# Kernel optimization log

Measured on AMD Instinct MI355X. Metric: run time of the kernel, lower is better.

Reference implementation:

```python
import jax, jax.numpy as jnp
import numpy as np

N = 100_000   # nodes
E = 1_600_000 # edges
IN, H, OUT = 128, 128, 128
G = 64        # graphs in batch
EPS = 1e-5    # batchnorm eps


def setup_inputs() -> dict:
    key = jax.random.key(0)
    ks = jax.random.split(key, 16)
    x = jax.random.normal(ks[0], (N, IN), dtype=jnp.float32)
    edge_index = jax.random.randint(ks[1], (2, E), 0, N, dtype=jnp.int32)
    batch = jnp.sort(jax.random.randint(ks[2], (N,), 0, G, dtype=jnp.int32))
    def lin(k, fi, fo):
        return jax.random.normal(k, (fi, fo), dtype=jnp.float32) / np.sqrt(fi).astype(np.float32)
    inp = {
        'x': x, 'edge_index': edge_index, 'batch': batch,
        'W1': lin(ks[3], IN, H), 'b1': jnp.zeros((H,), jnp.float32),
        'g1': jnp.ones((H,), jnp.float32), 'beta1': jnp.zeros((H,), jnp.float32),
        'W2': lin(ks[4], H, H), 'b2': jnp.zeros((H,), jnp.float32),
        'g2': jnp.ones((H,), jnp.float32), 'beta2': jnp.zeros((H,), jnp.float32),
        'W3': lin(ks[5], H, H), 'b3': jnp.zeros((H,), jnp.float32),
        'g3': jnp.ones((H,), jnp.float32), 'beta3': jnp.zeros((H,), jnp.float32),
        'fc_w': lin(ks[6], H, OUT), 'fc_b': jnp.zeros((OUT,), jnp.float32),
    }
    return inp


def _gcn_prep(edge_index):
    # add self loops, compute symmetric normalization (shared across layers)
    loop = jnp.arange(N, dtype=edge_index.dtype)
    row = jnp.concatenate([edge_index[0], loop])  # source
    col = jnp.concatenate([edge_index[1], loop])  # target
    deg = jax.ops.segment_sum(jnp.ones_like(col, dtype=jnp.float32), col, num_segments=N)
    dinv = jnp.where(deg > 0, jax.lax.rsqrt(deg), 0.0)
    norm = dinv[row] * dinv[col]  # (E+N,)
    return row, col, norm


def _gcn_bn_relu(h, W, b, g, beta, row, col, norm):
    hw = h @ W                                           # (N, H)
    msg = norm[:, None] * hw[row]                        # gather + scale
    h = jax.ops.segment_sum(msg, col, num_segments=N) + b  # scatter-add
    # BatchNorm1d (training-mode batch statistics, biased var)
    mu = jnp.mean(h, axis=0)
    var = jnp.mean(jnp.square(h - mu), axis=0)
    h = g * (h - mu) * jax.lax.rsqrt(var + EPS) + beta
    return jax.nn.relu(h)


def reference(x, edge_index, batch, W1, b1, g1, beta1, W2, b2, g2, beta2,
              W3, b3, g3, beta3, fc_w, fc_b):
    row, col, norm = _gcn_prep(edge_index)
    h = _gcn_bn_relu(x, W1, b1, g1, beta1, row, col, norm)
    h = _gcn_bn_relu(h, W2, b2, g2, beta2, row, col, norm)
    h = _gcn_bn_relu(h, W3, b3, g3, beta3, row, col, norm)
    # global_mean_pool over batch assignment
    sums = jax.ops.segment_sum(h, batch, num_segments=G)
    cnt = jax.ops.segment_sum(jnp.ones((N,), jnp.float32), batch, num_segments=G)
    pooled = sums / jnp.maximum(cnt, 1.0)[:, None]       # (G, H)
    return pooled @ fc_w + fc_b                          # (G, OUT)
```

## Files before the change

### kernel.cpp

```cpp
#include <hip/hip_runtime.h>

#define NN 100000
#define EE 1600000
#define HH 128
#define GG 64
#define TOT (EE + NN)
#define PSPLIT 8
#define NB 782
#define BCAP 4096
#define FCHUNK 4096

typedef __attribute__((ext_vector_type(8))) short s16x8;
typedef __attribute__((ext_vector_type(4))) float f32x4;

__device__ __forceinline__ unsigned short f2bf(float f) {
    unsigned u = __float_as_uint(f);
    u = u + 0x7FFFu + ((u >> 16) & 1u);
    return (unsigned short)(u >> 16);
}


__global__ __launch_bounds__(256) void setup_kernel(const float* __restrict__ x,
                                                    const int* __restrict__ batch,
                                                    const float* __restrict__ W0,
                                                    const float* __restrict__ W1,
                                                    const float* __restrict__ W2,
                                                    unsigned* __restrict__ Xbf,
                                                    int* __restrict__ cursor,
                                                    int* __restrict__ gstart, int* __restrict__ gend,
                                                    float* __restrict__ poolsum,
                                                    unsigned short* __restrict__ Wt) {
    int i = blockIdx.x * 256 + threadIdx.x;
    if (i < NN * 64) {
        float2 v = ((const float2*)x)[i];
        Xbf[i] = (unsigned)f2bf(v.x) | ((unsigned)f2bf(v.y) << 16);
    }
    if (i < NB) cursor[i] = i * BCAP;
    if (i < GG * HH) poolsum[i] = 0.f;
    if (i < GG) {
        int lo = 0, hi = NN;
        while (lo < hi) { int m = (lo + hi) >> 1; if (batch[m] < i) lo = m + 1; else hi = m; }
        int s = lo;
        lo = 0; hi = NN;
        while (lo < hi) { int m = (lo + hi) >> 1; if (batch[m] < i + 1) lo = m + 1; else hi = m; }
        gstart[i] = s;
        gend[i] = lo;
    }
    if (i < 3 * HH * HH) {
        int l = i >> 14, r = i & 16383;
        const float* W = (l == 0) ? W0 : (l == 1) ? W1 : W2;
        int k = r >> 7, n = r & 127;
        Wt[l * HH * HH + n * HH + k] = f2bf(W[r]);
    }
}

__global__ __launch_bounds__(256) void bfill2_kernel(const int* __restrict__ ei, int* cursor,
                                                     unsigned* __restrict__ ebuf) {
    __shared__ int h[NB];
    __shared__ int lbase[NB];
    int tid = threadIdx.x;
    size_t e0 = (size_t)blockIdx.x * FCHUNK;
    for (int i = tid; i < NB; i += 256) h[i] = 0;
    __syncthreads();
    unsigned r[16], c[16];
#pragma unroll
    for (int k = 0; k < 16; ++k) {
        size_t e = e0 + (size_t)k * 256 + tid;
        unsigned rr = 0xFFFFFFFFu, cc = 0;
        if (e < EE) {
            rr = (unsigned)ei[e];
            cc = (unsigned)ei[EE + e];
            if (rr >= NN || cc >= NN) rr = 0xFFFFFFFFu;
        }
        r[k] = rr; c[k] = cc;
        if (rr != 0xFFFFFFFFu) atomicAdd(&h[cc >> 7], 1);
    }
    __syncthreads();
    for (int i = tid; i < NB; i += 256) {
        int cnt = h[i];
        lbase[i] = cnt ? atomicAdd(&cursor[i], cnt) : 0;
    }
    __syncthreads();
    for (int i = tid; i < NB; i += 256) h[i] = 0;
    __syncthreads();
#pragma unroll
    for (int k = 0; k < 16; ++k) {
        if (r[k] != 0xFFFFFFFFu) {
            unsigned cc = c[k];
            int b = cc >> 7;
            int slot = lbase[b] + atomicAdd(&h[b], 1);
            if (slot >= b * BCAP && slot < (b + 1) * BCAP)
                ebuf[slot] = (r[k] << 7) | (cc & 127u);
        }
    }
}

__global__ void bscan_kernel(const int* __restrict__ cursor, int* __restrict__ bucketSlotStart,
                             int* __restrict__ col_start) {
    __shared__ int ss[1024];
    int t = threadIdx.x;
    int ec = 0, nc = 0;
    if (t < NB) {
        ec = min(max(cursor[t] - t * BCAP, 0), BCAP);
        nc = min(128, NN - t * 128);
    }
    ss[t] = ec + nc;
    __syncthreads();
    for (int off = 1; off < 1024; off <<= 1) {
        int a = 0;
        if (t >= off) a = ss[t - off];
        __syncthreads();
        ss[t] += a;
        __syncthreads();
    }
    if (t < NB) bucketSlotStart[t] = ss[t] - (ec + nc);
    if (t == NB - 1) col_start[NN] = ss[t];
}

__global__ __launch_bounds__(256) void bproc_kernel(const unsigned* __restrict__ ebuf,
                                                    const int* __restrict__ cursor,
                                                    const int* __restrict__ bucketSlotStart,
                                                    int* __restrict__ col_start,
                                                    float* __restrict__ dinv,
                                                    int* __restrict__ srcv) {
    __shared__ unsigned s_e[BCAP];
    __shared__ int s_cnt[128], s_scan[128], s_cur[128];
    int b = blockIdx.x;
    int tid = threadIdx.x;
    int n0 = b * 128;
    int nb = min(128, NN - n0);
    int est = b * BCAP;
    int ecnt = min(max(cursor[b] - est, 0), BCAP);
    if (tid < 128) s_cnt[tid] = 0;
    __syncthreads();
    for (int i = tid; i < ecnt; i += 256) {
        unsigned v = ebuf[est + i];
        s_e[i] = v;
        atomicAdd(&s_cnt[v & 127u], 1);
    }
    __syncthreads();
    int myc = 0;
    if (tid < 128) {
        myc = (tid < nb) ? s_cnt[tid] + 1 : 0;
        s_scan[tid] = myc;
    }
    __syncthreads();
    for (int off = 1; off < 128; off <<= 1) {
        int a = 0;
        if (tid < 128 && tid >= off) a = s_scan[tid - off];
        __syncthreads();
        if (tid < 128) s_scan[tid] += a;
        __syncthreads();
    }
    if (tid < nb) {
        int slotbase = bucketSlotStart[b] + s_scan[tid] - myc;
        col_start[n0 + tid] = slotbase;
        dinv[n0 + tid] = rsqrtf((float)(s_cnt[tid] + 1));
        srcv[slotbase] = n0 + tid;
        s_cur[tid] = slotbase + 1;
    }
    __syncthreads();
    for (int i = tid; i < ecnt; i += 256) {
        unsigned v = s_e[i];
        int slot = atomicAdd(&s_cur[v & 127u], 1);
        srcv[slot] = (int)(v >> 7);
    }
}


__global__ __launch_bounds__(256) void agg_kernel(const uint4* __restrict__ Xbf4,
                                                  const int* __restrict__ col_start,
                                                  const int* __restrict__ srcv,
                                                  const float* __restrict__ dinv,
                                                  unsigned short* __restrict__ Abf,
                                                  float* __restrict__ gsum,
                                                  float* __restrict__ gsq) {
    if (blockIdx.x == 0 && threadIdx.x < HH) {
        gsum[threadIdx.x] = 0.f;
        gsq[threadIdx.x] = 0.f;
    }
    int wid = (int)((blockIdx.x * blockDim.x + threadIdx.x) >> 6);
    int lane = threadIdx.x & 63;
    if (wid >= NN) return;
    int s0 = col_start[wid], s1 = col_start[wid + 1];
    float dd = dinv[wid];
    int q = lane >> 4;
    int l16 = lane & 15;
    float acc[8];
#pragma unroll
    for (int j = 0; j < 8; ++j) acc[j] = 0.f;

    for (int base = s0; base < s1; base += 64) {
        int cnt = min(64, s1 - base);
        int msrc = 0;
        float mw = 0.f;
        if (lane < cnt) { msrc = srcv[base + lane]; mw = dinv[msrc] * dd; }
        int rounds = (cnt + 3) >> 2;
        int p = 0;
        for (; p + 4 <= rounds; p += 4) {
            uint4 u[4];
            float w[4];
#pragma unroll
            for (int k = 0; k < 4; ++k) {
                int idx = (p + k) * 4 + q;
                int src = __shfl(msrc, idx);
                w[k] = __shfl(mw, idx);
                u[k] = Xbf4[(size_t)src * 16 + l16];
            }
#pragma unroll
            for (int k = 0; k < 4; ++k) {
                acc[0] += w[k] * __uint_as_float(u[k].x << 16);
                acc[1] += w[k] * __uint_as_float(u[k].x & 0xFFFF0000u);
                acc[2] += w[k] * __uint_as_float(u[k].y << 16);
                acc[3] += w[k] * __uint_as_float(u[k].y & 0xFFFF0000u);
                acc[4] += w[k] * __uint_as_float(u[k].z << 16);
                acc[5] += w[k] * __uint_as_float(u[k].z & 0xFFFF0000u);
                acc[6] += w[k] * __uint_as_float(u[k].w << 16);
                acc[7] += w[k] * __uint_as_float(u[k].w & 0xFFFF0000u);
            }
        }
        for (; p < rounds; ++p) {
            int idx = p * 4 + q;
            int src = __shfl(msrc, idx);
            float w = __shfl(mw, idx);
            uint4 u = Xbf4[(size_t)src * 16 + l16];
            acc[0] += w * __uint_as_float(u.x << 16);
            acc[1] += w * __uint_as_float(u.x & 0xFFFF0000u);
            acc[2] += w * __uint_as_float(u.y << 16);
            acc[3] += w * __uint_as_float(u.y & 0xFFFF0000u);
            acc[4] += w * __uint_as_float(u.z << 16);
            acc[5] += w * __uint_as_float(u.z & 0xFFFF0000u);
            acc[6] += w * __uint_as_float(u.w << 16);
            acc[7] += w * __uint_as_float(u.w & 0xFFFF0000u);
        }
    }
#pragma unroll
    for (int j = 0; j < 8; ++j) {
        acc[j] += __shfl_xor(acc[j], 16);
        acc[j] += __shfl_xor(acc[j], 32);
    }
    if (q == 0) {
        uint4 pk;
        pk.x = (unsigned)f2bf(acc[0]) | ((unsigned)f2bf(acc[1]) << 16);
        pk.y = (unsigned)f2bf(acc[2]) | ((unsigned)f2bf(acc[3]) << 16);
        pk.z = (unsigned)f2bf(acc[4]) | ((unsigned)f2bf(acc[5]) << 16);
        pk.w = (unsigned)f2bf(acc[6]) | ((unsigned)f2bf(acc[7]) << 16);
        ((uint4*)Abf)[(size_t)wid * 16 + l16] = pk;
    }
}

__global__ __launch_bounds__(256) void gemm_stats_kernel(unsigned short* __restrict__ Abf,
                                                         const unsigned short* __restrict__ Wt,
                                                         const float* __restrict__ bias,
                                                         float* __restrict__ gsum,
                                                         float* __restrict__ gsq) {
    __shared__ unsigned short wlds[128 * 136];
    __shared__ float ssum[HH], ssq[HH];
    int tid = threadIdx.x;
    if (tid < HH) { ssum[tid] = 0.f; ssq[tid] = 0.f; }
#pragma unroll
    for (int it = 0; it < 16; ++it) {
        int idx = it * 256 + tid;
        int r = idx >> 5, c = idx & 31;
        *(uint2*)&wlds[r * 136 + c * 4] = *(const uint2*)(Wt + r * HH + c * 4);
    }
    __syncthreads();

    int lane = tid & 63;
    int wave = tid >> 6;
    int mcol = lane & 15;
    int quad = lane >> 4;
    int rowbase = blockIdx.x * 128 + wave * 32;
    int row0 = rowbase + mcol;
    int row1 = row0 + 16;

    f32x4 acc[2][8];
#pragma unroll
    for (int mt = 0; mt < 2; ++mt)
#pragma unroll
        for (int nt = 0; nt < 8; ++nt) acc[mt][nt] = (f32x4){0.f, 0.f, 0.f, 0.f};

    s16x8 zf = {0, 0, 0, 0, 0, 0, 0, 0};
#pragma unroll
    for (int ks = 0; ks < 4; ++ks) {
        int k0 = ks * 32 + quad * 8;
        s16x8 a0 = (row0 < NN) ? *(const s16x8*)(Abf + (size_t)row0 * HH + k0) : zf;
        s16x8 a1 = (row1 < NN) ? *(const s16x8*)(Abf + (size_t)row1 * HH + k0) : zf;
#pragma unroll
        for (int nt = 0; nt < 8; ++nt) {
            s16x8 b = *(const s16x8*)&wlds[(nt * 16 + mcol) * 136 + k0];
            acc[0][nt] = __builtin_amdgcn_mfma_f32_16x16x32_bf16(a0, b, acc[0][nt], 0, 0, 0);
            acc[1][nt] = __builtin_amdgcn_mfma_f32_16x16x32_bf16(a1, b, acc[1][nt], 0, 0, 0);
        }
    }

    float s[8], sq[8];
#pragma unroll
    for (int nt = 0; nt < 8; ++nt) { s[nt] = 0.f; sq[nt] = 0.f; }
#pragma unroll
    for (int mt = 0; mt < 2; ++mt) {
        int rbase = rowbase + mt * 16 + quad * 4;
#pragma unroll
        for (int nt = 0; nt < 8; ++nt) {
            int col = nt * 16 + mcol;
            float bv = bias[col];
            f32x4 a = acc[mt][nt];
#pragma unroll
            for (int reg = 0; reg < 4; ++reg) {
                int r = rbase + reg;
                if (r < NN) {
                    float h = a[reg] + bv;
                    Abf[(size_t)r * HH + col] = f2bf(h);
                    s[nt] += h; sq[nt] += h * h;
                }
            }
        }
    }
#pragma unroll
    for (int nt = 0; nt < 8; ++nt) {
        float v = s[nt];  v += __shfl_xor(v, 16);  v += __shfl_xor(v, 32);
        float w = sq[nt]; w += __shfl_xor(w, 16);  w += __shfl_xor(w, 32);
        if (quad == 0) {
            atomicAdd(&ssum[nt * 16 + mcol], v);
            atomicAdd(&ssq[nt * 16 + mcol], w);
        }
    }
    __syncthreads();
    if (tid < HH) {
        atomicAdd(&gsum[tid], ssum[tid]);
        atomicAdd(&gsq[tid], ssq[tid]);
    }
}

__global__ __launch_bounds__(256) void apply_kernel(const unsigned short* __restrict__ Hb,
                                                    const float* __restrict__ gsum,
                                                    const float* __restrict__ gsq,
                                                    const float* __restrict__ g,
                                                    const float* __restrict__ beta,
                                                    unsigned short* __restrict__ Xb16) {
    __shared__ float asc[HH], bsh[HH];
    int tid = threadIdx.x;
    if (tid < HH) {
        float mu = gsum[tid] * (1.f / (float)NN);
        float var = fmaxf(gsq[tid] * (1.f / (float)NN) - mu * mu, 0.f);
        float a = g[tid] * rsqrtf(var + 1e-5f);
        asc[tid] = a;
        bsh[tid] = beta[tid] - a * mu;
    }
    __syncthreads();
    int i = blockIdx.x * 256 + tid;
    if (i >= NN * 16) return;
    int c8 = (i & 15) * 8;
    uint4 u = ((const uint4*)Hb)[i];
    unsigned w[4] = {u.x, u.y, u.z, u.w};
    unsigned r[4];
#pragma unroll
    for (int k = 0; k < 4; ++k) {
        int c = c8 + 2 * k;
        float h0 = __uint_as_float(w[k] << 16);
        float h1 = __uint_as_float(w[k] & 0xFFFF0000u);
        float o0 = fmaxf(asc[c] * h0 + bsh[c], 0.f);
        float o1 = fmaxf(asc[c + 1] * h1 + bsh[c + 1], 0.f);
        r[k] = (unsigned)f2bf(o0) | ((unsigned)f2bf(o1) << 16);
    }
    uint4 o;
    o.x = r[0]; o.y = r[1]; o.z = r[2]; o.w = r[3];
    ((uint4*)Xb16)[i] = o;
}


__global__ void pool_kernel(const unsigned* __restrict__ Xbf, const int* __restrict__ gstart,
                            const int* __restrict__ gend, float* __restrict__ poolsum) {
    int g = blockIdx.x;
    int sp = blockIdx.y;
    int t = threadIdx.x;
    int s = gstart[g], e = gend[g];
    if (e <= s) return;
    int len = e - s;
    int chunk = (len + PSPLIT - 1) / PSPLIT;
    int cs = s + sp * chunk;
    int ce = min(cs + chunk, e);
    if (cs >= ce) return;
    float2 acc = make_float2(0.f, 0.f);
    for (int i = cs; i < ce; ++i) {
        unsigned u = Xbf[(size_t)i * 64 + t];
        acc.x += __uint_as_float(u << 16);
        acc.y += __uint_as_float(u & 0xFFFF0000u);
    }
    atomicAdd(&poolsum[g * HH + 2 * t], acc.x);
    atomicAdd(&poolsum[g * HH + 2 * t + 1], acc.y);
}

__global__ void fc_kernel(const float* __restrict__ poolsum, const int* __restrict__ gstart,
                          const int* __restrict__ gend, const float* __restrict__ fc_w,
                          const float* __restrict__ fc_b, float* __restrict__ out) {
    int g = blockIdx.x;
    int o = threadIdx.x;
    int cnt = gend[g] - gstart[g];
    float inv = (cnt > 0) ? (1.f / (float)cnt) : 0.f;
    float acc = fc_b[o];
    for (int k = 0; k < HH; ++k) acc += (poolsum[g * HH + k] * inv) * fc_w[k * HH + o];
    out[g * HH + o] = acc;
}


extern "C" void kernel_launch(void* const* d_in, const int* in_sizes, int n_in,
                              void* d_out, int out_size, void* d_ws, size_t ws_size,
                              hipStream_t stream) {
    const float* x     = (const float*)d_in[0];
    const int*   ei    = (const int*)d_in[1];
    const int*   batch = (const int*)d_in[2];
    const float* Wl[3]    = {(const float*)d_in[3], (const float*)d_in[7], (const float*)d_in[11]};
    const float* bl[3]    = {(const float*)d_in[4], (const float*)d_in[8], (const float*)d_in[12]};
    const float* gl[3]    = {(const float*)d_in[5], (const float*)d_in[9], (const float*)d_in[13]};
    const float* betal[3] = {(const float*)d_in[6], (const float*)d_in[10], (const float*)d_in[14]};
    const float* fc_w = (const float*)d_in[15];
    const float* fc_b = (const float*)d_in[16];
    float* out = (float*)d_out;

    char* ws = (char*)d_ws;
    size_t off = 0;
    auto take = [&](size_t n) -> void* {
        void* p = ws + off;
        off = (off + n + 255) & ~(size_t)255;
        return p;
    };
    int*   bucketSlotStart = (int*)take((size_t)NB * 4);
    int*   cursor          = (int*)take((size_t)NB * 4);
    unsigned* ebuf         = (unsigned*)take((size_t)NB * BCAP * 4);
    int*   col_start       = (int*)take((size_t)(NN + 1) * 4);
    float* dinv            = (float*)take((size_t)NN * 4);
    int*   srcv            = (int*)take((size_t)TOT * 4);
    float* gsum            = (float*)take(HH * 4);
    float* gsq             = (float*)take(HH * 4);
    int*   gstart          = (int*)take(GG * 4);
    int*   gend            = (int*)take(GG * 4);
    float* poolsum         = (float*)take((size_t)GG * HH * 4);
    unsigned short* wt     = (unsigned short*)take((size_t)3 * HH * HH * 2);
    unsigned* Xbf          = (unsigned*)take((size_t)NN * 64 * 4);
    unsigned short* Abf    = (unsigned short*)take((size_t)NN * HH * 2);

    setup_kernel<<<(NN * 64 + 255) / 256, 256, 0, stream>>>(x, batch, Wl[0], Wl[1], Wl[2],
                                                            Xbf, cursor, gstart, gend, poolsum, wt);
    bfill2_kernel<<<(EE + FCHUNK - 1) / FCHUNK, 256, 0, stream>>>(ei, cursor, ebuf);
    bscan_kernel<<<1, 1024, 0, stream>>>(cursor, bucketSlotStart, col_start);
    bproc_kernel<<<NB, 256, 0, stream>>>(ebuf, cursor, bucketSlotStart, col_start, dinv, srcv);

    for (int l = 0; l < 3; ++l) {
        const unsigned short* W = wt + (size_t)l * HH * HH;
        agg_kernel<<<(NN * 64 + 255) / 256, 256, 0, stream>>>((const uint4*)Xbf, col_start, srcv,
                                                              dinv, Abf, gsum, gsq);
        gemm_stats_kernel<<<(NN + 127) / 128, 256, 0, stream>>>(Abf, W, bl[l], gsum, gsq);
        apply_kernel<<<(NN * 16 + 255) / 256, 256, 0, stream>>>(Abf, gsum, gsq,
                                                                gl[l], betal[l],
                                                                (unsigned short*)Xbf);
    }

    pool_kernel<<<dim3(GG, PSPLIT), 64, 0, stream>>>(Xbf, gstart, gend, poolsum);
    fc_kernel<<<GG, 128, 0, stream>>>(poolsum, gstart, gend, fc_w, fc_b, out);
}
```

Before: 585.5 us.

## Recompute GEMM in fused BN-apply kernel and process two nodes per wave in aggregation

The aggregation kernel now has each 64-lane wave handle two destination nodes, 32 lanes each, and unrolls the gather six deep instead of four. This targets idle lanes on low-degree nodes and raises loads in flight. The stats GEMM no longer writes its pre-norm output. A new gemm_apply kernel recomputes the same GEMM and applies BatchNorm and ReLU in its epilogue, removing one bf16 write and read of the N×128 activation. The price is doing the MFMA GEMM twice per layer.

```diff
diff --git a/kernel.cpp b/kernel.cpp
--- a/kernel.cpp
+++ b/kernel.cpp
@@ -179,36 +179,41 @@
         gsum[threadIdx.x] = 0.f;
         gsq[threadIdx.x] = 0.f;
     }
-    int wid = (int)((blockIdx.x * blockDim.x + threadIdx.x) >> 6);
+    int wv = (int)((blockIdx.x * blockDim.x + threadIdx.x) >> 6);
     int lane = threadIdx.x & 63;
-    if (wid >= NN) return;
-    int s0 = col_start[wid], s1 = col_start[wid + 1];
-    float dd = dinv[wid];
-    int q = lane >> 4;
+    int half = lane >> 5;
+    int node = 2 * wv + half;
+    if (2 * wv >= NN) return;
+    bool valid = node < NN;
+    int s0 = 0, s1 = 0;
+    float dd = 0.f;
+    if (valid) { s0 = col_start[node]; s1 = col_start[node + 1]; dd = dinv[node]; }
+    int lane31 = lane & 31;
+    int qh = (lane >> 4) & 1;
     int l16 = lane & 15;
     float acc[8];
 #pragma unroll
     for (int j = 0; j < 8; ++j) acc[j] = 0.f;
 
-    for (int base = s0; base < s1; base += 64) {
-        int cnt = min(64, s1 - base);
+    for (int base = s0; base < s1; base += 32) {
+        int cnt = min(32, s1 - base);
         int msrc = 0;
         float mw = 0.f;
-        if (lane < cnt) { msrc = srcv[base + lane]; mw = dinv[msrc] * dd; }
-        int rounds = (cnt + 3) >> 2;
+        if (lane31 < cnt) { msrc = srcv[base + lane31]; mw = dinv[msrc] * dd; }
+        int rounds = (cnt + 1) >> 1;
         int p = 0;
-        for (; p + 4 <= rounds; p += 4) {
-            uint4 u[4];
-            float w[4];
-#pragma unroll
-            for (int k = 0; k < 4; ++k) {
-                int idx = (p + k) * 4 + q;
-                int src = __shfl(msrc, idx);
-                w[k] = __shfl(mw, idx);
+        for (; p + 6 <= rounds; p += 6) {
+            uint4 u[6];
+            float w[6];
+#pragma unroll
+            for (int k = 0; k < 6; ++k) {
+                int sl = half * 32 + (p + k) * 2 + qh;
+                int src = __shfl(msrc, sl);
+                w[k] = __shfl(mw, sl);
                 u[k] = Xbf4[(size_t)src * 16 + l16];
             }
 #pragma unroll
-            for (int k = 0; k < 4; ++k) {
+            for (int k = 0; k < 6; ++k) {
                 acc[0] += w[k] * __uint_as_float(u[k].x << 16);
                 acc[1] += w[k] * __uint_as_float(u[k].x & 0xFFFF0000u);
                 acc[2] += w[k] * __uint_as_float(u[k].y << 16);
@@ -220,9 +225,9 @@
             }
         }
         for (; p < rounds; ++p) {
-            int idx = p * 4 + q;
-            int src = __shfl(msrc, idx);
-            float w = __shfl(mw, idx);
+            int sl = half * 32 + p * 2 + qh;
+            int src = __shfl(msrc, sl);
+            float w = __shfl(mw, sl);
             uint4 u = Xbf4[(size_t)src * 16 + l16];
             acc[0] += w * __uint_as_float(u.x << 16);
             acc[1] += w * __uint_as_float(u.x & 0xFFFF0000u);
@@ -235,21 +240,18 @@
         }
     }
 #pragma unroll
-    for (int j = 0; j < 8; ++j) {
-        acc[j] += __shfl_xor(acc[j], 16);
-        acc[j] += __shfl_xor(acc[j], 32);
-    }
-    if (q == 0) {
+    for (int j = 0; j < 8; ++j) acc[j] += __shfl_xor(acc[j], 16);
+    if ((lane & 16) == 0 && valid) {
         uint4 pk;
         pk.x = (unsigned)f2bf(acc[0]) | ((unsigned)f2bf(acc[1]) << 16);
         pk.y = (unsigned)f2bf(acc[2]) | ((unsigned)f2bf(acc[3]) << 16);
         pk.z = (unsigned)f2bf(acc[4]) | ((unsigned)f2bf(acc[5]) << 16);
         pk.w = (unsigned)f2bf(acc[6]) | ((unsigned)f2bf(acc[7]) << 16);
-        ((uint4*)Abf)[(size_t)wid * 16 + l16] = pk;
-    }
-}
-
-__global__ __launch_bounds__(256) void gemm_stats_kernel(unsigned short* __restrict__ Abf,
+        ((uint4*)Abf)[(size_t)node * 16 + l16] = pk;
+    }
+}
+
+__global__ __launch_bounds__(256) void gemm_stats_kernel(const unsigned short* __restrict__ Abf,
                                                          const unsigned short* __restrict__ Wt,
                                                          const float* __restrict__ bias,
                                                          float* __restrict__ gsum,
@@ -302,15 +304,12 @@
         int rbase = rowbase + mt * 16 + quad * 4;
 #pragma unroll
         for (int nt = 0; nt < 8; ++nt) {
-            int col = nt * 16 + mcol;
-            float bv = bias[col];
+            float bv = bias[nt * 16 + mcol];
             f32x4 a = acc[mt][nt];
 #pragma unroll
             for (int reg = 0; reg < 4; ++reg) {
-                int r = rbase + reg;
-                if (r < NN) {
+                if (rbase + reg < NN) {
                     float h = a[reg] + bv;
-                    Abf[(size_t)r * HH + col] = f2bf(h);
                     s[nt] += h; sq[nt] += h * h;
                 }
             }
@@ -332,40 +331,78 @@
     }
 }
 
-__global__ __launch_bounds__(256) void apply_kernel(const unsigned short* __restrict__ Hb,
-                                                    const float* __restrict__ gsum,
-                                                    const float* __restrict__ gsq,
-                                                    const float* __restrict__ g,
-                                                    const float* __restrict__ beta,
-                                                    unsigned short* __restrict__ Xb16) {
+__global__ __launch_bounds__(256) void gemm_apply_kernel(const unsigned short* __restrict__ Abf,
+                                                         const unsigned short* __restrict__ Wt,
+                                                         const float* __restrict__ bias,
+                                                         const float* __restrict__ gsum,
+                                                         const float* __restrict__ gsq,
+                                                         const float* __restrict__ g,
+                                                         const float* __restrict__ beta,
+                                                         unsigned short* __restrict__ Xb16) {
+    __shared__ unsigned short wlds[128 * 136];
     __shared__ float asc[HH], bsh[HH];
     int tid = threadIdx.x;
+#pragma unroll
+    for (int it = 0; it < 16; ++it) {
+        int idx = it * 256 + tid;
+        int r = idx >> 5, c = idx & 31;
+        *(uint2*)&wlds[r * 136 + c * 4] = *(const uint2*)(Wt + r * HH + c * 4);
+    }
     if (tid < HH) {
         float mu = gsum[tid] * (1.f / (float)NN);
         float var = fmaxf(gsq[tid] * (1.f / (float)NN) - mu * mu, 0.f);
         float a = g[tid] * rsqrtf(var + 1e-5f);
         asc[tid] = a;
-        bsh[tid] = beta[tid] - a * mu;
-    }
-    __syncthreads();
-    int i = blockIdx.x * 256 + tid;
-    if (i >= NN * 16) return;
-    int c8 = (i & 15) * 8;
-    uint4 u = ((const uint4*)Hb)[i];
-    unsigned w[4] = {u.x, u.y, u.z, u.w};
-    unsigned r[4];
-#pragma unroll
-    for (int k = 0; k < 4; ++k) {
-        int c = c8 + 2 * k;
-        float h0 = __uint_as_float(w[k] << 16);
-        float h1 = __uint_as_float(w[k] & 0xFFFF0000u);
-        float o0 = fmaxf(asc[c] * h0 + bsh[c], 0.f);
-        float o1 = fmaxf(asc[c + 1] * h1 + bsh[c + 1], 0.f);
-        r[k] = (unsigned)f2bf(o0) | ((unsigned)f2bf(o1) << 16);
-    }
-    uint4 o;
-    o.x = r[0]; o.y = r[1]; o.z = r[2]; o.w = r[3];
-    ((uint4*)Xb16)[i] = o;
+        bsh[tid] = a * (bias[tid] - mu) + beta[tid];
+    }
+    __syncthreads();
+
+    int lane = tid & 63;
+    int wave = tid >> 6;
+    int mcol = lane & 15;
+    int quad = lane >> 4;
+    int rowbase = blockIdx.x * 128 + wave * 32;
+    int row0 = rowbase + mcol;
+    int row1 = row0 + 16;
+
+    f32x4 acc[2][8];
+#pragma unroll
+    for (int mt = 0; mt < 2; ++mt)
+#pragma unroll
+        for (int nt = 0; nt < 8; ++nt) acc[mt][nt] = (f32x4){0.f, 0.f, 0.f, 0.f};
+
+    s16x8 zf = {0, 0, 0, 0, 0, 0, 0, 0};
+#pragma unroll
+    for (int ks = 0; ks < 4; ++ks) {
+        int k0 = ks * 32 + quad * 8;
+        s16x8 a0 = (row0 < NN) ? *(const s16x8*)(Abf + (size_t)row0 * HH + k0) : zf;
+        s16x8 a1 = (row1 < NN) ? *(const s16x8*)(Abf + (size_t)row1 * HH + k0) : zf;
+#pragma unroll
+        for (int nt = 0; nt < 8; ++nt) {
+            s16x8 b = *(const s16x8*)&wlds[(nt * 16 + mcol) * 136 + k0];
+            acc[0][nt] = __builtin_amdgcn_mfma_f32_16x16x32_bf16(a0, b, acc[0][nt], 0, 0, 0);
+            acc[1][nt] = __builtin_amdgcn_mfma_f32_16x16x32_bf16(a1, b, acc[1][nt], 0, 0, 0);
+        }
+    }
+
+#pragma unroll
+    for (int mt = 0; mt < 2; ++mt) {
+        int rbase = rowbase + mt * 16 + quad * 4;
+#pragma unroll
+        for (int nt = 0; nt < 8; ++nt) {
+            int col = nt * 16 + mcol;
+            float av = asc[col], bv = bsh[col];
+            f32x4 a = acc[mt][nt];
+#pragma unroll
+            for (int reg = 0; reg < 4; ++reg) {
+                int r = rbase + reg;
+                if (r < NN) {
+                    float o = fmaxf(av * a[reg] + bv, 0.f);
+                    Xb16[(size_t)r * HH + col] = f2bf(o);
+                }
+            }
+        }
+    }
 }
 
 
@@ -446,12 +483,13 @@
     bscan_kernel<<<1, 1024, 0, stream>>>(cursor, bucketSlotStart, col_start);
     bproc_kernel<<<NB, 256, 0, stream>>>(ebuf, cursor, bucketSlotStart, col_start, dinv, srcv);
 
+    const int aggBlocks = (((NN + 1) / 2) * 64 + 255) / 256;
     for (int l = 0; l < 3; ++l) {
         const unsigned short* W = wt + (size_t)l * HH * HH;
-        agg_kernel<<<(NN * 64 + 255) / 256, 256, 0, stream>>>((const uint4*)Xbf, col_start, srcv,
-                                                              dinv, Abf, gsum, gsq);
+        agg_kernel<<<aggBlocks, 256, 0, stream>>>((const uint4*)Xbf, col_start, srcv,
+                                                  dinv, Abf, gsum, gsq);
         gemm_stats_kernel<<<(NN + 127) / 128, 256, 0, stream>>>(Abf, W, bl[l], gsum, gsq);
-        apply_kernel<<<(NN * 16 + 255) / 256, 256, 0, stream>>>(Abf, gsum, gsq,
+        gemm_apply_kernel<<<(NN + 127) / 128, 256, 0, stream>>>(Abf, W, bl[l], gsum, gsq,
                                                                 gl[l], betal[l],
                                                                 (unsigned short*)Xbf);
     }
```

Result: faster. 555.4 us (-5.1%).
